# Performance work log

Hardware: AMD Instinct MI355X
Metric: run time of the kernel (lower is better)

## Reference

```python
import jax, jax.numpy as jnp
import numpy as np

LN_EPS = 1e-5
GRID_MIN, GRID_MAX = -1.0, 1.0


def make_grid(grid_size: int, spline_order: int) -> jnp.ndarray:
    h = (GRID_MAX - GRID_MIN) / grid_size
    # extended knot vector: grid_size + 2*spline_order + 1 knots
    return (jnp.arange(-spline_order, grid_size + spline_order + 1, dtype=jnp.float32) * h
            + GRID_MIN)


def b_splines(x: jnp.ndarray, grid: jnp.ndarray, k: int) -> jnp.ndarray:
    """Cox-de Boor B-spline bases. x: [B, in] -> [B, in, grid_size + k]."""
    x = x[..., None]  # [B, in, 1]
    bases = ((x >= grid[:-1]) & (x < grid[1:])).astype(x.dtype)
    for p in range(1, k + 1):
        left = (x - grid[: -(p + 1)]) / (grid[p:-1] - grid[: -(p + 1)]) * bases[..., :-1]
        right = (grid[p + 1:] - x) / (grid[p + 1:] - grid[1:-p]) * bases[..., 1:]
        bases = left + right
    return bases  # [B, in, grid_size + k]


def kan_layer(x, base_w, spline_w, grid, k):
    # base path: silu(x) @ base_w.T ; spline path: einsum over basis functions
    base = jnp.einsum('bi,oi->bo', jax.nn.silu(x), base_w)
    spl = jnp.einsum('big,oig->bo', b_splines(x, grid, k), spline_w)
    return base + spl


def layer_norm(x, gamma, beta):
    mu = jnp.mean(x, axis=-1, keepdims=True)
    var = jnp.mean(jnp.square(x - mu), axis=-1, keepdims=True)
    return (x - mu) * jax.lax.rsqrt(var + LN_EPS) * gamma + beta


def setup_inputs() -> dict:
    key = jax.random.key(0)
    ks = jax.random.split(key, 6)
    B, S, H, A = 32768, 256, 512, 64
    G, K = 5, 3
    nb = G + K  # 8 basis functions per edge
    s = 0.1
    return {
        'state': jax.random.normal(ks[0], (B, S), dtype=jnp.float32),
        'feat_base_w': jax.random.normal(ks[1], (H, S), dtype=jnp.float32) * s,
        'feat_spline_w': jax.random.normal(ks[2], (H, S, nb), dtype=jnp.float32) * s,
        'ln_gamma': jnp.ones((H,), dtype=jnp.float32),
        'ln_beta': jnp.zeros((H,), dtype=jnp.float32),
        'mean_base_w': jax.random.normal(ks[3], (A, H), dtype=jnp.float32) * s,
        'mean_spline_w': jax.random.normal(ks[4], (A, H, nb), dtype=jnp.float32) * s,
        'lstd_base_w': jax.random.normal(ks[5], (A, H), dtype=jnp.float32) * s,
        'lstd_spline_w': jax.random.normal(jax.random.fold_in(key, 7), (A, H, nb), dtype=jnp.float32) * s,
        'grid_size': G,
        'spline_order': K,
    }


def reference(state, feat_base_w, feat_spline_w, ln_gamma, ln_beta,
              mean_base_w, mean_spline_w, lstd_base_w, lstd_spline_w,
              grid_size, spline_order):
    LOG_STD_MIN, LOG_STD_MAX = -20.0, 2.0
    grid = make_grid(grid_size, spline_order)
    x = kan_layer(state, feat_base_w, feat_spline_w, grid, spline_order)
    x = jax.nn.relu(layer_norm(x, ln_gamma, ln_beta))
    mean = jnp.tanh(kan_layer(x, mean_base_w, mean_spline_w, grid, spline_order))
    log_std = jnp.clip(kan_layer(x, lstd_base_w, lstd_spline_w, grid, spline_order),
                       LOG_STD_MIN, LOG_STD_MAX)
    return mean, log_std
```

## Files before the change

### kernel.cpp

```cpp
#include <hip/hip_runtime.h>
#include <stdint.h>

typedef __bf16 bf16x8 __attribute__((ext_vector_type(8)));
typedef float f32x4 __attribute__((ext_vector_type(4)));
typedef unsigned short u16x8 __attribute__((ext_vector_type(8)));
typedef unsigned int as1_uint __attribute__((address_space(1)));
typedef unsigned int as3_uint __attribute__((address_space(3)));

#define N_B 32768
#define S_IN 256
#define H_DIM 512
#define A_DIM 64
#define K1_DIM 2304
#define K2_DIM 4608

static __device__ __forceinline__ unsigned short f2bf(float f) {
  union { float f; unsigned u; } v; v.f = f;
  unsigned r = v.u + 0x7fffu + ((v.u >> 16) & 1u);
  return (unsigned short)(r >> 16);
}

static __device__ __forceinline__ void gload_lds16(const void* g, void* l) {
  __builtin_amdgcn_global_load_lds((const as1_uint*)g, (as3_uint*)l, 16, 0, 0);
}

static __device__ __forceinline__ void bspline_w(float x, float& c,
    float& w0, float& w1, float& w2, float& w3) {
  float u = fmaf(2.5f, x, 5.5f);
  c = floorf(u);
  float f = u - c;
  float f2 = f * f;
  float f3 = f2 * f;
  const float k6 = 1.f / 6.f;
  w3 = f3 * k6;
  w2 = (3.f * (f + f2 - f3) + 1.f) * k6;
  w1 = (3.f * f3 - 6.f * f2 + 4.f) * k6;
  float omf = 1.f - f;
  w0 = omf * omf * omf * k6;
}

static __device__ __forceinline__ float silu_f(float x) {
  return x / (1.f + __expf(-x));
}

__global__ void k_sentinel(float* out, int n) {
  int i = blockIdx.x * blockDim.x + threadIdx.x;
  for (; i < n; i += gridDim.x * blockDim.x) out[i] = 12345.f;
}

__global__ void k_prep_w1(const float* __restrict__ base_w,
                          const float* __restrict__ spline_w,
                          unsigned short* __restrict__ W1) {
  int idx = blockIdx.x * blockDim.x + threadIdx.x;
  int n = idx / K1_DIM;
  int k = idx - n * K1_DIM;
  int j = k >> 8;
  int i = k & 255;
  float v = (j == 0) ? base_w[n * S_IN + i]
                     : spline_w[(size_t)(n * S_IN + i) * 8 + (j - 1)];
  W1[idx] = f2bf(v);
}

__global__ void k_prep_w2(const float* __restrict__ mean_base,
                          const float* __restrict__ mean_spl,
                          const float* __restrict__ lstd_base,
                          const float* __restrict__ lstd_spl,
                          unsigned short* __restrict__ W2) {
  int idx = blockIdx.x * blockDim.x + threadIdx.x;
  int n = idx / K2_DIM;
  int k = idx - n * K2_DIM;
  int j = k >> 9;
  int h = k & 511;
  const float* bw = (n < 64) ? mean_base : lstd_base;
  const float* sw = (n < 64) ? mean_spl : lstd_spl;
  int nn = n & 63;
  float v = (j == 0) ? bw[nn * H_DIM + h]
                     : sw[(size_t)(nn * H_DIM + h) * 8 + (j - 1)];
  W2[idx] = f2bf(v);
}

__global__ void k_features1(const float* __restrict__ state,
                            unsigned short* __restrict__ F1) {
  int tid = blockIdx.x * blockDim.x + threadIdx.x;
  int base = tid * 4;
  int b = base >> 8;
  int i = base & 255;
  const float4 xv = *(const float4*)(state + base);
  float xs[4] = {xv.x, xv.y, xv.z, xv.w};
  unsigned short outj[9][4];
  #pragma unroll
  for (int e = 0; e < 4; ++e) {
    float x = xs[e];
    float c, w0, w1, w2, w3;
    bspline_w(x, c, w0, w1, w2, w3);
    outj[0][e] = f2bf(silu_f(x));
    #pragma unroll
    for (int g = 0; g < 8; ++g) {
      float d = c - (float)g;
      float v = 0.f;
      v = (d == 0.f) ? w3 : v;
      v = (d == 1.f) ? w2 : v;
      v = (d == 2.f) ? w1 : v;
      v = (d == 3.f) ? w0 : v;
      outj[g + 1][e] = f2bf(v);
    }
  }
  size_t rowbase = (size_t)b * K1_DIM + i;
  #pragma unroll
  for (int j = 0; j < 9; ++j) {
    *(ushort4*)(F1 + rowbase + j * S_IN) =
        make_ushort4(outj[j][0], outj[j][1], outj[j][2], outj[j][3]);
  }
}

__global__ __launch_bounds__(256, 2) void k_gemm1(
    const unsigned short* __restrict__ F1,
    const unsigned short* __restrict__ W1,
    float* __restrict__ X) {
  extern __shared__ unsigned short smem[];
  unsigned short* As0 = smem;
  unsigned short* As1 = smem + 8192;
  unsigned short* Bs0 = smem + 16384;
  unsigned short* Bs1 = smem + 24576;

  const int t = threadIdx.x;
  const int bm = blockIdx.x >> 2;
  const int bn = blockIdx.x & 3;

  const unsigned short* Ab = F1 + (size_t)bm * 128 * K1_DIM;
  const unsigned short* Bb = W1 + (size_t)bn * 128 * K1_DIM;

  const int srow = t >> 3;
  const int scol = (t & 7) * 8;

  auto stage = [&](int buf, int kt) {
    unsigned short* Ad = buf ? As1 : As0;
    unsigned short* Bd = buf ? Bs1 : Bs0;
    const size_t k0 = (size_t)kt * 64;
    #pragma unroll
    for (int q = 0; q < 4; ++q) {
      const int r = q * 32 + srow;
      gload_lds16(Ab + (size_t)r * K1_DIM + k0 + scol, Ad + r * 64 + scol);
      gload_lds16(Bb + (size_t)r * K1_DIM + k0 + scol, Bd + r * 64 + scol);
    }
  };

  const int wave = t >> 6;
  const int lane = t & 63;
  const int wm = (wave >> 1) * 64;
  const int wn = (wave & 1) * 64;
  const int lr = lane & 15;
  const int lk = (lane >> 4) * 8;

  f32x4 acc[4][4];
  #pragma unroll
  for (int i = 0; i < 4; ++i)
    #pragma unroll
    for (int jj = 0; jj < 4; ++jj)
      acc[i][jj] = (f32x4){0.f, 0.f, 0.f, 0.f};

  stage(0, 0);
  __syncthreads();
  int cur = 0;
  const int NT = K1_DIM / 64;
  for (int kt = 0; kt < NT; ++kt) {
    if (kt + 1 < NT) stage(cur ^ 1, kt + 1);
    const unsigned short* A0 = cur ? As1 : As0;
    const unsigned short* B0 = cur ? Bs1 : Bs0;
    #pragma unroll
    for (int ks = 0; ks < 2; ++ks) {
      bf16x8 af[4], bfv[4];
      #pragma unroll
      for (int fm = 0; fm < 4; ++fm)
        af[fm] = *(const bf16x8*)(A0 + (wm + fm * 16 + lr) * 64 + ks * 32 + lk);
      #pragma unroll
      for (int fn = 0; fn < 4; ++fn)
        bfv[fn] = *(const bf16x8*)(B0 + (wn + fn * 16 + lr) * 64 + ks * 32 + lk);
      #pragma unroll
      for (int fm = 0; fm < 4; ++fm)
        #pragma unroll
        for (int fn = 0; fn < 4; ++fn)
          acc[fm][fn] = __builtin_amdgcn_mfma_f32_16x16x32_bf16(
              af[fm], bfv[fn], acc[fm][fn], 0, 0, 0);
    }
    __syncthreads();
    cur ^= 1;
  }

  float* Xb = X + (size_t)bm * 128 * H_DIM + bn * 128;
  #pragma unroll
  for (int fm = 0; fm < 4; ++fm) {
    const int row0 = wm + fm * 16 + (lane >> 4) * 4;
    #pragma unroll
    for (int fn = 0; fn < 4; ++fn) {
      const int col = wn + fn * 16 + lr;
      #pragma unroll
      for (int r = 0; r < 4; ++r)
        Xb[(size_t)(row0 + r) * H_DIM + col] = acc[fm][fn][r];
    }
  }
}

__global__ __launch_bounds__(256, 2) void k_gemm2(
    const float* __restrict__ X, const unsigned short* __restrict__ W2,
    const float* __restrict__ gamma, const float* __restrict__ beta,
    float* __restrict__ out) {
  extern __shared__ unsigned short smem2[];
  unsigned short* At = smem2;
  unsigned short* Bt = smem2 + 64 * 64;

  const int t = threadIdx.x;
  const int bm = blockIdx.x;
  const int row = t >> 2;
  const int quart = t & 3;
  const int wave = t >> 6;
  const int lane = t & 63;
  const int wn = wave * 32;
  const int lr = lane & 15;
  const int lk = (lane >> 4) * 8;

  const float* Xrow = X + (size_t)(bm * 64 + row) * H_DIM;

  float s = 0.f, ss = 0.f;
  #pragma unroll 4
  for (int q = 0; q < 32; ++q) {
    float4 v = *(const float4*)(Xrow + quart * 128 + q * 4);
    s += v.x + v.y + v.z + v.w;
    ss += v.x * v.x + v.y * v.y + v.z * v.z + v.w * v.w;
  }
  s += __shfl_xor(s, 1); ss += __shfl_xor(ss, 1);
  s += __shfl_xor(s, 2); ss += __shfl_xor(ss, 2);
  const float mu = s * (1.f / 512.f);
  const float var = ss * (1.f / 512.f) - mu * mu;
  const float rstd = rsqrtf(var + 1e-5f);

  f32x4 acc[4][2];
  #pragma unroll
  for (int i = 0; i < 4; ++i)
    #pragma unroll
    for (int jj = 0; jj < 2; ++jj)
      acc[i][jj] = (f32x4){0.f, 0.f, 0.f, 0.f};

  float cw[16], w0[16], w1[16], w2[16], w3[16];

  const int sbrow = t >> 3;
  const int sbcol = (t & 7) * 8;

  for (int hb = 0; hb < 8; ++hb) {
    for (int j = 0; j < 9; ++j) {
      __syncthreads();
      {
        const size_t k0 = (size_t)j * 512 + hb * 64;
        #pragma unroll
        for (int q = 0; q < 4; ++q) {
          const int r = q * 32 + sbrow;
          gload_lds16(W2 + (size_t)r * K2_DIM + k0 + sbcol, Bt + r * 64 + sbcol);
        }
      }
      unsigned short av[16];
      if (j == 0) {
        #pragma unroll
        for (int c4 = 0; c4 < 4; ++c4) {
          const int h = hb * 64 + quart * 16 + c4 * 4;
          const float4 xv = *(const float4*)(Xrow + h);
          const float4 gv = *(const float4*)(gamma + h);
          const float4 bv = *(const float4*)(beta + h);
          float xa[4] = {xv.x, xv.y, xv.z, xv.w};
          float ga[4] = {gv.x, gv.y, gv.z, gv.w};
          float ba[4] = {bv.x, bv.y, bv.z, bv.w};
          #pragma unroll
          for (int e2 = 0; e2 < 4; ++e2) {
            const int e = c4 * 4 + e2;
            float xn = fmaf((xa[e2] - mu) * rstd, ga[e2], ba[e2]);
            xn = fmaxf(xn, 0.f);
            bspline_w(xn, cw[e], w0[e], w1[e], w2[e], w3[e]);
            av[e] = f2bf(silu_f(xn));
          }
        }
      } else {
        const float g = (float)(j - 1);
        #pragma unroll
        for (int e = 0; e < 16; ++e) {
          const float d = cw[e] - g;
          float v = 0.f;
          v = (d == 0.f) ? w3[e] : v;
          v = (d == 1.f) ? w2[e] : v;
          v = (d == 2.f) ? w1[e] : v;
          v = (d == 3.f) ? w0[e] : v;
          av[e] = f2bf(v);
        }
      }
      u16x8 p0, p1;
      #pragma unroll
      for (int e = 0; e < 8; ++e) { p0[e] = av[e]; p1[e] = av[e + 8]; }
      *(u16x8*)(At + row * 64 + quart * 16) = p0;
      *(u16x8*)(At + row * 64 + quart * 16 + 8) = p1;

      __syncthreads();

      #pragma unroll
      for (int ks = 0; ks < 2; ++ks) {
        bf16x8 af[4], bfv[2];
        #pragma unroll
        for (int fm = 0; fm < 4; ++fm)
          af[fm] = *(const bf16x8*)(At + (fm * 16 + lr) * 64 + ks * 32 + lk);
        #pragma unroll
        for (int fn = 0; fn < 2; ++fn)
          bfv[fn] = *(const bf16x8*)(Bt + (wn + fn * 16 + lr) * 64 + ks * 32 + lk);
        #pragma unroll
        for (int fm = 0; fm < 4; ++fm)
          #pragma unroll
          for (int fn = 0; fn < 2; ++fn)
            acc[fm][fn] = __builtin_amdgcn_mfma_f32_16x16x32_bf16(
                af[fm], bfv[fn], acc[fm][fn], 0, 0, 0);
      }
    }
  }

  float* mean_out = out;
  float* lstd_out = out + (size_t)N_B * A_DIM;
  #pragma unroll
  for (int fm = 0; fm < 4; ++fm) {
    const int r0 = bm * 64 + fm * 16 + (lane >> 4) * 4;
    #pragma unroll
    for (int fn = 0; fn < 2; ++fn) {
      const int n = wn + fn * 16 + lr;
      #pragma unroll
      for (int r = 0; r < 4; ++r) {
        const float v = acc[fm][fn][r];
        if (n < 64) mean_out[(size_t)(r0 + r) * 64 + n] = tanhf(v);
        else lstd_out[(size_t)(r0 + r) * 64 + (n - 64)] = fminf(fmaxf(v, -20.f), 2.f);
      }
    }
  }
}

extern "C" void kernel_launch(void* const* d_in, const int* in_sizes, int n_in,
                              void* d_out, int out_size, void* d_ws, size_t ws_size,
                              hipStream_t stream) {
  const float* state         = (const float*)d_in[0];
  const float* feat_base_w   = (const float*)d_in[1];
  const float* feat_spline_w = (const float*)d_in[2];
  const float* ln_gamma      = (const float*)d_in[3];
  const float* ln_beta       = (const float*)d_in[4];
  const float* mean_base_w   = (const float*)d_in[5];
  const float* mean_spline_w = (const float*)d_in[6];
  const float* lstd_base_w   = (const float*)d_in[7];
  const float* lstd_spline_w = (const float*)d_in[8];

  const size_t W1_OFF = 0;
  const size_t W2_OFF = 2359296;
  const size_t F1_OFF = 3538944;
  const size_t X_OFF  = 154533888;
  const size_t NEED   = 221642752;

  if (ws_size < NEED) {
    hipLaunchKernelGGL(k_sentinel, dim3(4096), dim3(256), 0, stream,
                       (float*)d_out, out_size);
    return;
  }

  char* ws = (char*)d_ws;
  unsigned short* W1 = (unsigned short*)(ws + W1_OFF);
  unsigned short* W2 = (unsigned short*)(ws + W2_OFF);
  unsigned short* F1 = (unsigned short*)(ws + F1_OFF);
  float* X = (float*)(ws + X_OFF);

  hipLaunchKernelGGL(k_prep_w1, dim3(4608), dim3(256), 0, stream,
                     feat_base_w, feat_spline_w, W1);
  hipLaunchKernelGGL(k_prep_w2, dim3(2304), dim3(256), 0, stream,
                     mean_base_w, mean_spline_w, lstd_base_w, lstd_spline_w, W2);
  hipLaunchKernelGGL(k_features1, dim3(8192), dim3(256), 0, stream, state, F1);
  hipLaunchKernelGGL(k_gemm1, dim3(1024), dim3(256), 65536, stream, F1, W1, X);
  hipLaunchKernelGGL(k_gemm2, dim3(512), dim3(256), 24576, stream,
                     X, W2, ln_gamma, ln_beta, (float*)d_out);
}
```

Measured before the change: 271.7 us.

## Fuse B-spline feature generation into GEMM1 and interleave K layout per input

Removes the separate feature kernel and its large bf16 F1 buffer. GEMM1 now computes silu and spline features in-register per 32-input chunk and writes them to LDS, using a sparse shift-based packing of the four nonzero basis weights. Both weight matrices are re-laid so that the nine features of each input sit next to each other along K, and both GEMMs read B fragments straight from global memory with register double-buffering instead of staging them in LDS. This saves roughly 150MB of HBM traffic, but B operands are now fetched from global/L2 per wave, and GEMM1 tiles shrink to 64x128 (2048 blocks), which may lower reuse.

```diff
diff --git a/kernel.cpp b/kernel.cpp
--- a/kernel.cpp
+++ b/kernel.cpp
@@ -3,16 +3,15 @@
 
 typedef __bf16 bf16x8 __attribute__((ext_vector_type(8)));
 typedef float f32x4 __attribute__((ext_vector_type(4)));
-typedef unsigned short u16x8 __attribute__((ext_vector_type(8)));
-typedef unsigned int as1_uint __attribute__((address_space(1)));
-typedef unsigned int as3_uint __attribute__((address_space(3)));
 
 #define N_B 32768
 #define S_IN 256
 #define H_DIM 512
-#define A_DIM 64
 #define K1_DIM 2304
 #define K2_DIM 4608
+#define LDA 296
+
+#define MFMA __builtin_amdgcn_mfma_f32_16x16x32_bf16
 
 static __device__ __forceinline__ unsigned short f2bf(float f) {
   union { float f; unsigned u; } v; v.f = f;
@@ -20,27 +19,51 @@
   return (unsigned short)(r >> 16);
 }
 
-static __device__ __forceinline__ void gload_lds16(const void* g, void* l) {
-  __builtin_amdgcn_global_load_lds((const as1_uint*)g, (as3_uint*)l, 16, 0, 0);
-}
-
-static __device__ __forceinline__ void bspline_w(float x, float& c,
-    float& w0, float& w1, float& w2, float& w3) {
+static __device__ __forceinline__ void kan_feat(float x, unsigned& s16,
+    unsigned& q0, unsigned& q1, unsigned& q2, unsigned& q3) {
+  s16 = f2bf(x / (1.f + __expf(-x)));
   float u = fmaf(2.5f, x, 5.5f);
-  c = floorf(u);
-  float f = u - c;
+  float cf = floorf(u);
+  float f = u - cf;
   float f2 = f * f;
   float f3 = f2 * f;
   const float k6 = 1.f / 6.f;
-  w3 = f3 * k6;
-  w2 = (3.f * (f + f2 - f3) + 1.f) * k6;
-  w1 = (3.f * f3 - 6.f * f2 + 4.f) * k6;
+  float w3v = f3 * k6;
+  float w2v = (3.f * (f + f2 - f3) + 1.f) * k6;
+  float w1v = (3.f * f3 - 6.f * f2 + 4.f) * k6;
   float omf = 1.f - f;
-  w0 = omf * omf * omf * k6;
-}
-
-static __device__ __forceinline__ float silu_f(float x) {
-  return x / (1.f + __expf(-x));
+  float w0v = omf * omf * omf * k6;
+  int i0 = (int)cf - 3;
+  uint64_t W64 = (uint64_t)((unsigned)f2bf(w0v) | ((unsigned)f2bf(w1v) << 16))
+               | ((uint64_t)((unsigned)f2bf(w2v) | ((unsigned)f2bf(w3v) << 16)) << 32);
+  uint64_t lo = 0, hi = 0;
+  if (i0 >= 0) {
+    int s = i0 * 16;
+    lo = (i0 < 4) ? (W64 << (s & 63)) : 0;
+    uint64_t hr = (i0 >= 1 && i0 < 4) ? (W64 >> ((64 - s) & 63)) : 0;
+    uint64_t hl = (i0 >= 4 && i0 < 8) ? (W64 << ((s - 64) & 63)) : 0;
+    hi = hr | hl;
+  } else {
+    lo = (i0 >= -3) ? (W64 >> ((-i0 * 16) & 63)) : 0;
+  }
+  q0 = (unsigned)lo; q1 = (unsigned)(lo >> 32);
+  q2 = (unsigned)hi; q3 = (unsigned)(hi >> 32);
+}
+
+static __device__ __forceinline__ void feat_pack9(const float* xs, unsigned* o) {
+  #pragma unroll
+  for (int pe = 0; pe < 4; ++pe) {
+    unsigned sA, a0, a1, a2, a3, sB, b0, b1, b2, b3;
+    kan_feat(xs[2 * pe], sA, a0, a1, a2, a3);
+    kan_feat(xs[2 * pe + 1], sB, b0, b1, b2, b3);
+    unsigned* op = o + pe * 9;
+    op[0] = sA | (a0 << 16);
+    op[1] = (a0 >> 16) | (a1 << 16);
+    op[2] = (a1 >> 16) | (a2 << 16);
+    op[3] = (a2 >> 16) | (a3 << 16);
+    op[4] = (a3 >> 16) | (sB << 16);
+    op[5] = b0; op[6] = b1; op[7] = b2; op[8] = b3;
+  }
 }
 
 __global__ void k_sentinel(float* out, int n) {
@@ -54,8 +77,8 @@
   int idx = blockIdx.x * blockDim.x + threadIdx.x;
   int n = idx / K1_DIM;
   int k = idx - n * K1_DIM;
-  int j = k >> 8;
-  int i = k & 255;
+  int i = k / 9;
+  int j = k - i * 9;
   float v = (j == 0) ? base_w[n * S_IN + i]
                      : spline_w[(size_t)(n * S_IN + i) * 8 + (j - 1)];
   W1[idx] = f2bf(v);
@@ -69,8 +92,8 @@
   int idx = blockIdx.x * blockDim.x + threadIdx.x;
   int n = idx / K2_DIM;
   int k = idx - n * K2_DIM;
-  int j = k >> 9;
-  int h = k & 511;
+  int h = k / 9;
+  int j = k - h * 9;
   const float* bw = (n < 64) ? mean_base : lstd_base;
   const float* sw = (n < 64) ? mean_spl : lstd_spl;
   int nn = n & 63;
@@ -79,143 +102,98 @@
   W2[idx] = f2bf(v);
 }
 
-__global__ void k_features1(const float* __restrict__ state,
-                            unsigned short* __restrict__ F1) {
-  int tid = blockIdx.x * blockDim.x + threadIdx.x;
-  int base = tid * 4;
-  int b = base >> 8;
-  int i = base & 255;
-  const float4 xv = *(const float4*)(state + base);
-  float xs[4] = {xv.x, xv.y, xv.z, xv.w};
-  unsigned short outj[9][4];
-  #pragma unroll
-  for (int e = 0; e < 4; ++e) {
-    float x = xs[e];
-    float c, w0, w1, w2, w3;
-    bspline_w(x, c, w0, w1, w2, w3);
-    outj[0][e] = f2bf(silu_f(x));
-    #pragma unroll
-    for (int g = 0; g < 8; ++g) {
-      float d = c - (float)g;
-      float v = 0.f;
-      v = (d == 0.f) ? w3 : v;
-      v = (d == 1.f) ? w2 : v;
-      v = (d == 2.f) ? w1 : v;
-      v = (d == 3.f) ? w0 : v;
-      outj[g + 1][e] = f2bf(v);
-    }
-  }
-  size_t rowbase = (size_t)b * K1_DIM + i;
-  #pragma unroll
-  for (int j = 0; j < 9; ++j) {
-    *(ushort4*)(F1 + rowbase + j * S_IN) =
-        make_ushort4(outj[j][0], outj[j][1], outj[j][2], outj[j][3]);
-  }
-}
-
-__global__ __launch_bounds__(256, 2) void k_gemm1(
-    const unsigned short* __restrict__ F1,
+__global__ __launch_bounds__(256) void k_gemm1(
+    const float* __restrict__ state,
     const unsigned short* __restrict__ W1,
     float* __restrict__ X) {
-  extern __shared__ unsigned short smem[];
-  unsigned short* As0 = smem;
-  unsigned short* As1 = smem + 8192;
-  unsigned short* Bs0 = smem + 16384;
-  unsigned short* Bs1 = smem + 24576;
-
+  extern __shared__ unsigned short At[];
   const int t = threadIdx.x;
   const int bm = blockIdx.x >> 2;
   const int bn = blockIdx.x & 3;
-
-  const unsigned short* Ab = F1 + (size_t)bm * 128 * K1_DIM;
-  const unsigned short* Bb = W1 + (size_t)bn * 128 * K1_DIM;
-
-  const int srow = t >> 3;
-  const int scol = (t & 7) * 8;
-
-  auto stage = [&](int buf, int kt) {
-    unsigned short* Ad = buf ? As1 : As0;
-    unsigned short* Bd = buf ? Bs1 : Bs0;
-    const size_t k0 = (size_t)kt * 64;
-    #pragma unroll
-    for (int q = 0; q < 4; ++q) {
-      const int r = q * 32 + srow;
-      gload_lds16(Ab + (size_t)r * K1_DIM + k0 + scol, Ad + r * 64 + scol);
-      gload_lds16(Bb + (size_t)r * K1_DIM + k0 + scol, Bd + r * 64 + scol);
-    }
-  };
-
-  const int wave = t >> 6;
-  const int lane = t & 63;
-  const int wm = (wave >> 1) * 64;
-  const int wn = (wave & 1) * 64;
+  const int row = t >> 2, quart = t & 3;
+  const int wave = t >> 6, lane = t & 63;
+  const int wm = (wave & 1) * 32;
+  const int wn = (wave >> 1) * 64;
   const int lr = lane & 15;
   const int lk = (lane >> 4) * 8;
 
-  f32x4 acc[4][4];
-  #pragma unroll
-  for (int i = 0; i < 4; ++i)
-    #pragma unroll
-    for (int jj = 0; jj < 4; ++jj)
-      acc[i][jj] = (f32x4){0.f, 0.f, 0.f, 0.f};
-
-  stage(0, 0);
-  __syncthreads();
-  int cur = 0;
-  const int NT = K1_DIM / 64;
-  for (int kt = 0; kt < NT; ++kt) {
-    if (kt + 1 < NT) stage(cur ^ 1, kt + 1);
-    const unsigned short* A0 = cur ? As1 : As0;
-    const unsigned short* B0 = cur ? Bs1 : Bs0;
-    #pragma unroll
-    for (int ks = 0; ks < 2; ++ks) {
-      bf16x8 af[4], bfv[4];
-      #pragma unroll
-      for (int fm = 0; fm < 4; ++fm)
-        af[fm] = *(const bf16x8*)(A0 + (wm + fm * 16 + lr) * 64 + ks * 32 + lk);
-      #pragma unroll
-      for (int fn = 0; fn < 4; ++fn)
-        bfv[fn] = *(const bf16x8*)(B0 + (wn + fn * 16 + lr) * 64 + ks * 32 + lk);
-      #pragma unroll
-      for (int fm = 0; fm < 4; ++fm)
+  const float* xp = state + (size_t)(bm * 64 + row) * S_IN + quart * 8;
+
+  const unsigned short* bptr[4];
+  #pragma unroll
+  for (int fn = 0; fn < 4; ++fn)
+    bptr[fn] = W1 + (size_t)(bn * 128 + wn + fn * 16 + lr) * K1_DIM + lk;
+
+  f32x4 acc[2][4];
+  #pragma unroll
+  for (int a = 0; a < 2; ++a)
+    #pragma unroll
+    for (int b = 0; b < 4; ++b) acc[a][b] = (f32x4){0.f, 0.f, 0.f, 0.f};
+
+  for (int ch = 0; ch < 8; ++ch) {
+    __syncthreads();
+    float xs[8];
+    {
+      const float4 v0 = *(const float4*)(xp + ch * 32);
+      const float4 v1 = *(const float4*)(xp + ch * 32 + 4);
+      xs[0] = v0.x; xs[1] = v0.y; xs[2] = v0.z; xs[3] = v0.w;
+      xs[4] = v1.x; xs[5] = v1.y; xs[6] = v1.z; xs[7] = v1.w;
+    }
+    unsigned o[36];
+    feat_pack9(xs, o);
+    unsigned* dst = (unsigned*)(At + row * LDA + quart * 72);
+    #pragma unroll
+    for (int i = 0; i < 9; ++i)
+      *(uint4*)(dst + 4 * i) = make_uint4(o[4*i], o[4*i+1], o[4*i+2], o[4*i+3]);
+    __syncthreads();
+
+    const size_t ko = (size_t)ch * 288;
+    bf16x8 bb[2][4];
+    #pragma unroll
+    for (int fn = 0; fn < 4; ++fn)
+      bb[0][fn] = *(const bf16x8*)(bptr[fn] + ko);
+    #pragma unroll
+    for (int ks = 0; ks < 9; ++ks) {
+      if (ks < 8) {
         #pragma unroll
         for (int fn = 0; fn < 4; ++fn)
-          acc[fm][fn] = __builtin_amdgcn_mfma_f32_16x16x32_bf16(
-              af[fm], bfv[fn], acc[fm][fn], 0, 0, 0);
-    }
-    __syncthreads();
-    cur ^= 1;
-  }
-
-  float* Xb = X + (size_t)bm * 128 * H_DIM + bn * 128;
-  #pragma unroll
-  for (int fm = 0; fm < 4; ++fm) {
-    const int row0 = wm + fm * 16 + (lane >> 4) * 4;
+          bb[(ks + 1) & 1][fn] = *(const bf16x8*)(bptr[fn] + ko + (ks + 1) * 32);
+      }
+      const bf16x8 af0 = *(const bf16x8*)(At + (wm + lr) * LDA + ks * 32 + lk);
+      const bf16x8 af1 = *(const bf16x8*)(At + (wm + 16 + lr) * LDA + ks * 32 + lk);
+      #pragma unroll
+      for (int fn = 0; fn < 4; ++fn) {
+        acc[0][fn] = MFMA(af0, bb[ks & 1][fn], acc[0][fn], 0, 0, 0);
+        acc[1][fn] = MFMA(af1, bb[ks & 1][fn], acc[1][fn], 0, 0, 0);
+      }
+    }
+  }
+
+  float* Xb = X + (size_t)(bm * 64) * H_DIM + bn * 128;
+  #pragma unroll
+  for (int fm = 0; fm < 2; ++fm) {
+    const int r0 = wm + fm * 16 + (lane >> 4) * 4;
     #pragma unroll
     for (int fn = 0; fn < 4; ++fn) {
       const int col = wn + fn * 16 + lr;
       #pragma unroll
       for (int r = 0; r < 4; ++r)
-        Xb[(size_t)(row0 + r) * H_DIM + col] = acc[fm][fn][r];
-    }
-  }
-}
-
-__global__ __launch_bounds__(256, 2) void k_gemm2(
+        Xb[(size_t)(r0 + r) * H_DIM + col] = acc[fm][fn][r];
+    }
+  }
+}
+
+__global__ __launch_bounds__(256) void k_gemm2(
     const float* __restrict__ X, const unsigned short* __restrict__ W2,
     const float* __restrict__ gamma, const float* __restrict__ beta,
     float* __restrict__ out) {
-  extern __shared__ unsigned short smem2[];
-  unsigned short* At = smem2;
-  unsigned short* Bt = smem2 + 64 * 64;
-
+  extern __shared__ unsigned short At[];
   const int t = threadIdx.x;
   const int bm = blockIdx.x;
-  const int row = t >> 2;
-  const int quart = t & 3;
-  const int wave = t >> 6;
-  const int lane = t & 63;
-  const int wn = wave * 32;
+  const int row = t >> 2, quart = t & 3;
+  const int wave = t >> 6, lane = t & 63;
+  const int wm = (wave & 1) * 32;
+  const int wn = (wave >> 1) * 64;
   const int lr = lane & 15;
   const int lk = (lane >> 4) * 8;
 
@@ -234,102 +212,80 @@
   const float var = ss * (1.f / 512.f) - mu * mu;
   const float rstd = rsqrtf(var + 1e-5f);
 
-  f32x4 acc[4][2];
-  #pragma unroll
-  for (int i = 0; i < 4; ++i)
-    #pragma unroll
-    for (int jj = 0; jj < 2; ++jj)
-      acc[i][jj] = (f32x4){0.f, 0.f, 0.f, 0.f};
-
-  float cw[16], w0[16], w1[16], w2[16], w3[16];
-
-  const int sbrow = t >> 3;
-  const int sbcol = (t & 7) * 8;
-
-  for (int hb = 0; hb < 8; ++hb) {
-    for (int j = 0; j < 9; ++j) {
-      __syncthreads();
-      {
-        const size_t k0 = (size_t)j * 512 + hb * 64;
+  const unsigned short* bptr[4];
+  #pragma unroll
+  for (int fn = 0; fn < 4; ++fn)
+    bptr[fn] = W2 + (size_t)(wn + fn * 16 + lr) * K2_DIM + lk;
+
+  f32x4 acc[2][4];
+  #pragma unroll
+  for (int a = 0; a < 2; ++a)
+    #pragma unroll
+    for (int b = 0; b < 4; ++b) acc[a][b] = (f32x4){0.f, 0.f, 0.f, 0.f};
+
+  for (int ch = 0; ch < 16; ++ch) {
+    __syncthreads();
+    const int h0 = ch * 32 + quart * 8;
+    float xs[8];
+    {
+      const float4 xv0 = *(const float4*)(Xrow + h0);
+      const float4 xv1 = *(const float4*)(Xrow + h0 + 4);
+      const float4 gv0 = *(const float4*)(gamma + h0);
+      const float4 gv1 = *(const float4*)(gamma + h0 + 4);
+      const float4 bv0 = *(const float4*)(beta + h0);
+      const float4 bv1 = *(const float4*)(beta + h0 + 4);
+      xs[0] = fmaxf(fmaf((xv0.x - mu) * rstd, gv0.x, bv0.x), 0.f);
+      xs[1] = fmaxf(fmaf((xv0.y - mu) * rstd, gv0.y, bv0.y), 0.f);
+      xs[2] = fmaxf(fmaf((xv0.z - mu) * rstd, gv0.z, bv0.z), 0.f);
+      xs[3] = fmaxf(fmaf((xv0.w - mu) * rstd, gv0.w, bv0.w), 0.f);
+      xs[4] = fmaxf(fmaf((xv1.x - mu) * rstd, gv1.x, bv1.x), 0.f);
+      xs[5] = fmaxf(fmaf((xv1.y - mu) * rstd, gv1.y, bv1.y), 0.f);
+      xs[6] = fmaxf(fmaf((xv1.z - mu) * rstd, gv1.z, bv1.z), 0.f);
+      xs[7] = fmaxf(fmaf((xv1.w - mu) * rstd, gv1.w, bv1.w), 0.f);
+    }
+    unsigned o[36];
+    feat_pack9(xs, o);
+    unsigned* dst = (unsigned*)(At + row * LDA + quart * 72);
+    #pragma unroll
+    for (int i = 0; i < 9; ++i)
+      *(uint4*)(dst + 4 * i) = make_uint4(o[4*i], o[4*i+1], o[4*i+2], o[4*i+3]);
+    __syncthreads();
+
+    const size_t ko = (size_t)ch * 288;
+    bf16x8 bb[2][4];
+    #pragma unroll
+    for (int fn = 0; fn < 4; ++fn)
+      bb[0][fn] = *(const bf16x8*)(bptr[fn] + ko);
+    #pragma unroll
+    for (int ks = 0; ks < 9; ++ks) {
+      if (ks < 8) {
         #pragma unroll
-        for (int q = 0; q < 4; ++q) {
-          const int r = q * 32 + sbrow;
-          gload_lds16(W2 + (size_t)r * K2_DIM + k0 + sbcol, Bt + r * 64 + sbcol);
-        }
-      }
-      unsigned short av[16];
-      if (j == 0) {
-        #pragma unroll
-        for (int c4 = 0; c4 < 4; ++c4) {
-          const int h = hb * 64 + quart * 16 + c4 * 4;
-          const float4 xv = *(const float4*)(Xrow + h);
-          const float4 gv = *(const float4*)(gamma + h);
-          const float4 bv = *(const float4*)(beta + h);
-          float xa[4] = {xv.x, xv.y, xv.z, xv.w};
-          float ga[4] = {gv.x, gv.y, gv.z, gv.w};
-          float ba[4] = {bv.x, bv.y, bv.z, bv.w};
-          #pragma unroll
-          for (int e2 = 0; e2 < 4; ++e2) {
-            const int e = c4 * 4 + e2;
-            float xn = fmaf((xa[e2] - mu) * rstd, ga[e2], ba[e2]);
-            xn = fmaxf(xn, 0.f);
-            bspline_w(xn, cw[e], w0[e], w1[e], w2[e], w3[e]);
-            av[e] = f2bf(silu_f(xn));
-          }
-        }
-      } else {
-        const float g = (float)(j - 1);
-        #pragma unroll
-        for (int e = 0; e < 16; ++e) {
-          const float d = cw[e] - g;
-          float v = 0.f;
-          v = (d == 0.f) ? w3[e] : v;
-          v = (d == 1.f) ? w2[e] : v;
-          v = (d == 2.f) ? w1[e] : v;
-          v = (d == 3.f) ? w0[e] : v;
-          av[e] = f2bf(v);
-        }
-      }
-      u16x8 p0, p1;
+        for (int fn = 0; fn < 4; ++fn)
+          bb[(ks + 1) & 1][fn] = *(const bf16x8*)(bptr[fn] + ko + (ks + 1) * 32);
+      }
+      const bf16x8 af0 = *(const bf16x8*)(At + (wm + lr) * LDA + ks * 32 + lk);
+      const bf16x8 af1 = *(const bf16x8*)(At + (wm + 16 + lr) * LDA + ks * 32 + lk);
       #pragma unroll
-      for (int e = 0; e < 8; ++e) { p0[e] = av[e]; p1[e] = av[e + 8]; }
-      *(u16x8*)(At + row * 64 + quart * 16) = p0;
-      *(u16x8*)(At + row * 64 + quart * 16 + 8) = p1;
-
-      __syncthreads();
-
-      #pragma unroll
-      for (int ks = 0; ks < 2; ++ks) {
-        bf16x8 af[4], bfv[2];
-        #pragma unroll
-        for (int fm = 0; fm < 4; ++fm)
-          af[fm] = *(const bf16x8*)(At + (fm * 16 + lr) * 64 + ks * 32 + lk);
-        #pragma unroll
-        for (int fn = 0; fn < 2; ++fn)
-          bfv[fn] = *(const bf16x8*)(Bt + (wn + fn * 16 + lr) * 64 + ks * 32 + lk);
-        #pragma unroll
-        for (int fm = 0; fm < 4; ++fm)
-          #pragma unroll
-          for (int fn = 0; fn < 2; ++fn)
-            acc[fm][fn] = __builtin_amdgcn_mfma_f32_16x16x32_bf16(
-                af[fm], bfv[fn], acc[fm][fn], 0, 0, 0);
+      for (int fn = 0; fn < 4; ++fn) {
+        acc[0][fn] = MFMA(af0, bb[ks & 1][fn], acc[0][fn], 0, 0, 0);
+        acc[1][fn] = MFMA(af1, bb[ks & 1][fn], acc[1][fn], 0, 0, 0);
       }
     }
   }
 
   float* mean_out = out;
-  float* lstd_out = out + (size_t)N_B * A_DIM;
-  #pragma unroll
-  for (int fm = 0; fm < 4; ++fm) {
-    const int r0 = bm * 64 + fm * 16 + (lane >> 4) * 4;
-    #pragma unroll
-    for (int fn = 0; fn < 2; ++fn) {
+  float* lstd_out = out + (size_t)N_B * 64;
+  #pragma unroll
+  for (int fm = 0; fm < 2; ++fm) {
+    const int r0 = bm * 64 + wm + fm * 16 + (lane >> 4) * 4;
+    #pragma unroll
+    for (int fn = 0; fn < 4; ++fn) {
       const int n = wn + fn * 16 + lr;
       #pragma unroll
       for (int r = 0; r < 4; ++r) {
         const float v = acc[fm][fn][r];
         if (n < 64) mean_out[(size_t)(r0 + r) * 64 + n] = tanhf(v);
-        else lstd_out[(size_t)(r0 + r) * 64 + (n - 64)] = fminf(fmaxf(v, -20.f), 2.f);
+        else        lstd_out[(size_t)(r0 + r) * 64 + (n - 64)] = fminf(fmaxf(v, -20.f), 2.f);
       }
     }
   }
@@ -350,9 +306,8 @@
 
   const size_t W1_OFF = 0;
   const size_t W2_OFF = 2359296;
-  const size_t F1_OFF = 3538944;
-  const size_t X_OFF  = 154533888;
-  const size_t NEED   = 221642752;
+  const size_t X_OFF  = 3538944;
+  const size_t NEED   = 70647808;
 
   if (ws_size < NEED) {
     hipLaunchKernelGGL(k_sentinel, dim3(4096), dim3(256), 0, stream,
@@ -363,15 +318,14 @@
   char* ws = (char*)d_ws;
   unsigned short* W1 = (unsigned short*)(ws + W1_OFF);
   unsigned short* W2 = (unsigned short*)(ws + W2_OFF);
-  unsigned short* F1 = (unsigned short*)(ws + F1_OFF);
   float* X = (float*)(ws + X_OFF);
 
   hipLaunchKernelGGL(k_prep_w1, dim3(4608), dim3(256), 0, stream,
                      feat_base_w, feat_spline_w, W1);
   hipLaunchKernelGGL(k_prep_w2, dim3(2304), dim3(256), 0, stream,
                      mean_base_w, mean_spline_w, lstd_base_w, lstd_spline_w, W2);
-  hipLaunchKernelGGL(k_features1, dim3(8192), dim3(256), 0, stream, state, F1);
-  hipLaunchKernelGGL(k_gemm1, dim3(1024), dim3(256), 65536, stream, F1, W1, X);
-  hipLaunchKernelGGL(k_gemm2, dim3(512), dim3(256), 24576, stream,
+  hipLaunchKernelGGL(k_gemm1, dim3(2048), dim3(256), 64 * LDA * 2, stream,
+                     state, W1, X);
+  hipLaunchKernelGGL(k_gemm2, dim3(512), dim3(256), 64 * LDA * 2, stream,
                      X, W2, ln_gamma, ln_beta, (float*)d_out);
 }
```

Result: slower. 479.2 us (+76.4%).

## Swizzle global/LDS layouts to kill LDS bank conflicts; remap GEMM1 block order

Applied to the files above, without the earlier changes.

The F1, W1 and W2 buffers are now written with an XOR swizzle of 8-element chunks keyed on the row. Because the direct global-to-LDS copies keep that layout, the MFMA fragment reads in LDS hit different banks instead of conflicting on the 64-element row stride. GEMM2's A tile, built on the fly, gets a padded stride of 72 instead. GEMM1 also remaps block IDs so blocks spread across XCDs differently, which may change L2 reuse of A and B tiles. The cost is a little extra index arithmetic, and the producer and consumer swizzles must stay consistent.

```diff
diff --git a/kernel.cpp b/kernel.cpp
--- a/kernel.cpp
+++ b/kernel.cpp
@@ -13,6 +13,9 @@
 #define A_DIM 64
 #define K1_DIM 2304
 #define K2_DIM 4608
+#define LDA2 72
+
+#define MFMA __builtin_amdgcn_mfma_f32_16x16x32_bf16
 
 static __device__ __forceinline__ unsigned short f2bf(float f) {
   union { float f; unsigned u; } v; v.f = f;
@@ -22,6 +25,10 @@
 
 static __device__ __forceinline__ void gload_lds16(const void* g, void* l) {
   __builtin_amdgcn_global_load_lds((const as1_uint*)g, (as3_uint*)l, 16, 0, 0);
+}
+
+static __device__ __forceinline__ int swz64(int c, int row) {
+  return (c & ~63) | ((((c >> 3) & 7) ^ (row & 7)) << 3) | (c & 7);
 }
 
 static __device__ __forceinline__ void bspline_w(float x, float& c,
@@ -53,7 +60,8 @@
                           unsigned short* __restrict__ W1) {
   int idx = blockIdx.x * blockDim.x + threadIdx.x;
   int n = idx / K1_DIM;
-  int k = idx - n * K1_DIM;
+  int c = idx - n * K1_DIM;
+  int k = swz64(c, n);
   int j = k >> 8;
   int i = k & 255;
   float v = (j == 0) ? base_w[n * S_IN + i]
@@ -68,9 +76,10 @@
                           unsigned short* __restrict__ W2) {
   int idx = blockIdx.x * blockDim.x + threadIdx.x;
   int n = idx / K2_DIM;
-  int k = idx - n * K2_DIM;
-  int j = k >> 9;
-  int h = k & 511;
+  int c = idx - n * K2_DIM;
+  int k = swz64(c, n);
+  int j = k / 512;
+  int h = k - j * 512;
   const float* bw = (n < 64) ? mean_base : lstd_base;
   const float* sw = (n < 64) ? mean_spl : lstd_spl;
   int nn = n & 63;
@@ -105,10 +114,11 @@
       outj[g + 1][e] = f2bf(v);
     }
   }
-  size_t rowbase = (size_t)b * K1_DIM + i;
+  size_t rowbase = (size_t)b * K1_DIM;
   #pragma unroll
   for (int j = 0; j < 9; ++j) {
-    *(ushort4*)(F1 + rowbase + j * S_IN) =
+    int c = swz64(j * S_IN + i, b);
+    *(ushort4*)(F1 + rowbase + c) =
         make_ushort4(outj[j][0], outj[j][1], outj[j][2], outj[j][3]);
   }
 }
@@ -124,8 +134,9 @@
   unsigned short* Bs1 = smem + 24576;
 
   const int t = threadIdx.x;
-  const int bm = blockIdx.x >> 2;
-  const int bn = blockIdx.x & 3;
+  const int bid = (int)(blockIdx.x & 7) * 128 + ((int)blockIdx.x >> 3);
+  const int bm = bid >> 2;
+  const int bn = bid & 3;
 
   const unsigned short* Ab = F1 + (size_t)bm * 128 * K1_DIM;
   const unsigned short* Bb = W1 + (size_t)bn * 128 * K1_DIM;
@@ -150,7 +161,7 @@
   const int wm = (wave >> 1) * 64;
   const int wn = (wave & 1) * 64;
   const int lr = lane & 15;
-  const int lk = (lane >> 4) * 8;
+  const int l4 = lane >> 4;
 
   f32x4 acc[4][4];
   #pragma unroll
@@ -171,17 +182,22 @@
     for (int ks = 0; ks < 2; ++ks) {
       bf16x8 af[4], bfv[4];
       #pragma unroll
+      for (int fm = 0; fm < 4; ++fm) {
+        const int r = wm + fm * 16 + lr;
+        const int slot = (ks * 4 + l4) ^ (r & 7);
+        af[fm] = *(const bf16x8*)(A0 + r * 64 + slot * 8);
+      }
+      #pragma unroll
+      for (int fn = 0; fn < 4; ++fn) {
+        const int r = wn + fn * 16 + lr;
+        const int slot = (ks * 4 + l4) ^ (r & 7);
+        bfv[fn] = *(const bf16x8*)(B0 + r * 64 + slot * 8);
+      }
+      #pragma unroll
       for (int fm = 0; fm < 4; ++fm)
-        af[fm] = *(const bf16x8*)(A0 + (wm + fm * 16 + lr) * 64 + ks * 32 + lk);
-      #pragma unroll
-      for (int fn = 0; fn < 4; ++fn)
-        bfv[fn] = *(const bf16x8*)(B0 + (wn + fn * 16 + lr) * 64 + ks * 32 + lk);
-      #pragma unroll
-      for (int fm = 0; fm < 4; ++fm)
         #pragma unroll
         for (int fn = 0; fn < 4; ++fn)
-          acc[fm][fn] = __builtin_amdgcn_mfma_f32_16x16x32_bf16(
-              af[fm], bfv[fn], acc[fm][fn], 0, 0, 0);
+          acc[fm][fn] = MFMA(af[fm], bfv[fn], acc[fm][fn], 0, 0, 0);
     }
     __syncthreads();
     cur ^= 1;
@@ -190,7 +206,7 @@
   float* Xb = X + (size_t)bm * 128 * H_DIM + bn * 128;
   #pragma unroll
   for (int fm = 0; fm < 4; ++fm) {
-    const int row0 = wm + fm * 16 + (lane >> 4) * 4;
+    const int row0 = wm + fm * 16 + l4 * 4;
     #pragma unroll
     for (int fn = 0; fn < 4; ++fn) {
       const int col = wn + fn * 16 + lr;
@@ -207,7 +223,7 @@
     float* __restrict__ out) {
   extern __shared__ unsigned short smem2[];
   unsigned short* At = smem2;
-  unsigned short* Bt = smem2 + 64 * 64;
+  unsigned short* Bt = smem2 + 64 * LDA2;
 
   const int t = threadIdx.x;
   const int bm = blockIdx.x;
@@ -217,7 +233,7 @@
   const int lane = t & 63;
   const int wn = wave * 32;
   const int lr = lane & 15;
-  const int lk = (lane >> 4) * 8;
+  const int l4 = lane >> 4;
 
   const float* Xrow = X + (size_t)(bm * 64 + row) * H_DIM;
 
@@ -293,8 +309,8 @@
       u16x8 p0, p1;
       #pragma unroll
       for (int e = 0; e < 8; ++e) { p0[e] = av[e]; p1[e] = av[e + 8]; }
-      *(u16x8*)(At + row * 64 + quart * 16) = p0;
-      *(u16x8*)(At + row * 64 + quart * 16 + 8) = p1;
+      *(u16x8*)(At + row * LDA2 + quart * 16) = p0;
+      *(u16x8*)(At + row * LDA2 + quart * 16 + 8) = p1;
 
       __syncthreads();
 
@@ -303,16 +319,18 @@
         bf16x8 af[4], bfv[2];
         #pragma unroll
         for (int fm = 0; fm < 4; ++fm)
-          af[fm] = *(const bf16x8*)(At + (fm * 16 + lr) * 64 + ks * 32 + lk);
-        #pragma unroll
-        for (int fn = 0; fn < 2; ++fn)
-          bfv[fn] = *(const bf16x8*)(Bt + (wn + fn * 16 + lr) * 64 + ks * 32 + lk);
+          af[fm] = *(const bf16x8*)(At + (fm * 16 + lr) * LDA2 + ks * 32 + l4 * 8);
+        #pragma unroll
+        for (int fn = 0; fn < 2; ++fn) {
+          const int r = wn + fn * 16 + lr;
+          const int slot = (ks * 4 + l4) ^ (r & 7);
+          bfv[fn] = *(const bf16x8*)(Bt + r * 64 + slot * 8);
+        }
         #pragma unroll
         for (int fm = 0; fm < 4; ++fm)
           #pragma unroll
           for (int fn = 0; fn < 2; ++fn)
-            acc[fm][fn] = __builtin_amdgcn_mfma_f32_16x16x32_bf16(
-                af[fm], bfv[fn], acc[fm][fn], 0, 0, 0);
+            acc[fm][fn] = MFMA(af[fm], bfv[fn], acc[fm][fn], 0, 0, 0);
       }
     }
   }
@@ -321,7 +339,7 @@
   float* lstd_out = out + (size_t)N_B * A_DIM;
   #pragma unroll
   for (int fm = 0; fm < 4; ++fm) {
-    const int r0 = bm * 64 + fm * 16 + (lane >> 4) * 4;
+    const int r0 = bm * 64 + fm * 16 + l4 * 4;
     #pragma unroll
     for (int fn = 0; fn < 2; ++fn) {
       const int n = wn + fn * 16 + lr;
@@ -372,6 +390,6 @@
                      mean_base_w, mean_spline_w, lstd_base_w, lstd_spline_w, W2);
   hipLaunchKernelGGL(k_features1, dim3(8192), dim3(256), 0, stream, state, F1);
   hipLaunchKernelGGL(k_gemm1, dim3(1024), dim3(256), 65536, stream, F1, W1, X);
-  hipLaunchKernelGGL(k_gemm2, dim3(512), dim3(256), 24576, stream,
-                     X, W2, ln_gamma, ln_beta, (float*)d_out);
-}
+  hipLaunchKernelGGL(k_gemm2, dim3(512), dim3(256), (64 * LDA2 + 128 * 64) * 2,
+                     stream, X, W2, ln_gamma, ln_beta, (float*)d_out);
+}
```

After: 233.6 us. 1.16x faster.
